# Performance work log

Measured on AMD Instinct MI355X. Metric: run time of the kernel, lower is better.

The kernel has to match this reference:

```python
import jax, jax.numpy as jnp
import numpy as np

STRIDES = (2, 2, 2, 2)
ALPHA = 1.0
NEG_SLOPE = 0.1


def _conv1d(h, w, b, stride):
    # h: (N, C, L), w: (O, I, K) -> (N, O, L_out), VALID padding
    out = jax.lax.conv_general_dilated(
        h, w, window_strides=(stride,), padding='VALID',
        dimension_numbers=('NCH', 'OIH', 'NCH'))
    return out + b[None, :, None]


def setup_inputs() -> dict:
    key = jax.random.key(0)
    ks = jax.random.split(key, 10)
    N, C, L = 256, 128, 1024
    k_sizes = (15, 12, 7, 4)
    inp = {'x': jax.random.normal(ks[0], (N, C, L), dtype=jnp.float32)}
    for i, k in enumerate(k_sizes):
        fan_in = C * k
        scale = 1.0 / np.sqrt(fan_in).astype(np.float32)
        inp[f'w{i+1}'] = jax.random.normal(ks[1 + 2 * i], (C, C, k), dtype=jnp.float32) * scale
        inp[f'b{i+1}'] = jax.random.normal(ks[2 + 2 * i], (C,), dtype=jnp.float32) * 0.01
    D = C * 59  # flattened encoder output: 1024->505->247->121->59
    inp['centers'] = jax.random.normal(ks[9], (64, D), dtype=jnp.float32)
    return inp


def reference(x, w1, b1, w2, b2, w3, b3, w4, b4, centers):
    ws = [(w1, b1), (w2, b2), (w3, b3), (w4, b4)]
    h = x
    for i, ((w, b), s) in enumerate(zip(ws, STRIDES)):
        h = _conv1d(h, w, b, s)
        if i != len(ws) - 1:
            h = jnp.where(h > 0, h, NEG_SLOPE * h)  # LeakyReLU(0.1)
    z = h.reshape(h.shape[0], -1)  # (N, D)
    # squared distances via norm expansion: ||z||^2 + ||c||^2 - 2 z.c
    d2 = (jnp.sum(z * z, axis=1, keepdims=True)
          + jnp.sum(centers * centers, axis=1)[None, :]
          - 2.0 * z @ centers.T)  # (N, K)
    q = 1.0 / (1.0 + d2 / ALPHA)
    q = q ** ((ALPHA + 1.0) / 2.0)
    q = q / jnp.sum(q, axis=1, keepdims=True)
    return q
```

## Files before the change

kernel.cpp:

```cpp
#include <hip/hip_runtime.h>

typedef __bf16 bf16;
typedef __bf16 bf16x4 __attribute__((ext_vector_type(4)));
typedef __bf16 bf16x8 __attribute__((ext_vector_type(8)));
typedef float f32x4 __attribute__((ext_vector_type(4)));

#define CCH 128

__global__ void k_prep_all(const float* __restrict__ w1, const float* __restrict__ w2,
                           const float* __restrict__ w3, const float* __restrict__ w4,
                           const float* __restrict__ cen,
                           bf16* __restrict__ o1, bf16* __restrict__ o2,
                           bf16* __restrict__ o3, bf16* __restrict__ o4,
                           bf16* __restrict__ cbp, float* __restrict__ cc) {
    __shared__ float red[256];
    int tid = threadIdx.x;
    if (blockIdx.x < 2432) {
        int idx = blockIdx.x * 256 + tid;
        const float* src; bf16* dst; int Kw; int r = idx;
        if (r < 15 * 16384) { src = w1; dst = o1; Kw = 15; }
        else if ((r -= 15 * 16384) < 12 * 16384) { src = w2; dst = o2; Kw = 12; }
        else if ((r -= 12 * 16384) < 7 * 16384) { src = w3; dst = o3; Kw = 7; }
        else if ((r -= 7 * 16384) < 4 * 16384) { src = w4; dst = o4; Kw = 4; }
        else return;
        int e = r & 7, lane = (r >> 3) & 63, og = (r >> 9) & 7, c = (r >> 12) & 3, kt = r >> 14;
        int o = og * 16 + (lane & 15);
        int i = c * 32 + (lane >> 4) * 8 + e;
        dst[r] = (bf16)src[(o * 128 + i) * Kw + kt];
    } else {
        int k = blockIdx.x - 2432;
        float s = 0.f;
        for (int idx = tid; idx < 64 * 128; idx += 256) {
            int l = idx >> 7;
            int o = idx & 127;
            float v = (l < 59) ? cen[k * 7552 + o * 59 + l] : 0.f;
            bf16 b = (bf16)v;
            cbp[(size_t)k * 64 * 128 + idx] = b;
            float fv = (float)b;
            s += fv * fv;
        }
        red[tid] = s;
        __syncthreads();
        for (int st = 128; st > 0; st >>= 1) {
            if (tid < st) red[tid] += red[tid + st];
            __syncthreads();
        }
        if (tid == 0) cc[k] = red[0];
    }
}

__global__ __launch_bounds__(256, 4) void k_conv1(
    const float* __restrict__ x, const bf16* __restrict__ wTp,
    const float* __restrict__ bias, bf16* __restrict__ out) {
    constexpr int KW = 15, LT = 128, PH = 2, OUT_ROWS = 512;
    constexpr int P = (LT - 1) * 2 + KW;
    constexpr int KC = 2;
    constexpr int RS = 64;
    constexpr int NLT = LT / 16;
    constexpr int ESE = 136;
    constexpr int SMELE = (P * RS > LT * ESE) ? P * RS : LT * ESE;
    constexpr int NJ = KW * KC;
    __shared__ __align__(16) bf16 smem[SMELE];

    const int n = blockIdx.y;
    const int l0 = blockIdx.x * LT;
    const int p0 = l0 * 2;
    const int tid = threadIdx.x;
    const int wid = tid >> 6;
    const int lane = tid & 63;
    const int quad = lane >> 4;
    const int l15 = lane & 15;
    const int og0 = wid * 2;

    f32x4 acc[2][NLT];
#pragma unroll
    for (int a = 0; a < 2; ++a)
#pragma unroll
        for (int b = 0; b < NLT; ++b) acc[a][b] = (f32x4){0.f, 0.f, 0.f, 0.f};

    bf16x8 afr[2][2];
    const bf16* wbase = wTp + (size_t)lane * 8;
    afr[0][0] = *(const bf16x8*)(wbase + ((size_t)(og0 + 0) << 9));
    afr[0][1] = *(const bf16x8*)(wbase + ((size_t)(og0 + 1) << 9));

    const int cst = tid >> 2;
    const int qw = tid & 3;

#pragma unroll 1
    for (int ph = 0; ph < PH; ++ph) {
        if (ph) __syncthreads();

        const float* bch = x + ((size_t)(n * 128 + ph * 64 + cst)) * 1024;
#pragma unroll 4
        for (int it = 0; it < 17; ++it) {
            int pp = it * 16 + qw * 4;
            int gp = p0 + pp;
            f32x4 t;
            if (gp + 3 < 1024) {
                t = *(const f32x4*)(bch + gp);
            } else {
#pragma unroll
                for (int e = 0; e < 4; ++e) t[e] = (gp + e < 1024) ? bch[gp + e] : 0.f;
            }
#pragma unroll
            for (int e = 0; e < 4; ++e) {
                int ppe = pp + e;
                int sc8 = (((cst >> 3) ^ ((ppe >> 1) & 7)) << 3) | (cst & 7);
                smem[ppe * RS + sc8] = (bf16)t[e];
            }
        }
        __syncthreads();

#pragma unroll 2
        for (int j = 0; j < NJ; ++j) {
            int nj = j + 1, nph = ph;
            if (nj == NJ) { nj = 0; ++nph; }
            if (nph < PH) {
                int kt1 = nj >> 1;
                int c1 = (nj & (KC - 1)) + nph * KC;
                const bf16* wp = wbase + ((size_t)((kt1 * 4 + c1) * 8 + og0) << 9);
                afr[(j + 1) & 1][0] = *(const bf16x8*)(wp);
                afr[(j + 1) & 1][1] = *(const bf16x8*)(wp + 512);
            }
            const int kt = j >> 1;
            const int c16l = (j & (KC - 1)) * 4 + quad;
#pragma unroll
            for (int lt = 0; lt < NLT; ++lt) {
                int p = (lt * 16 + l15) * 2 + kt;
                int sc = c16l ^ ((p >> 1) & 7);
                bf16x8 bfr = *(const bf16x8*)(smem + p * RS + sc * 8);
                acc[0][lt] = __builtin_amdgcn_mfma_f32_16x16x32_bf16(
                    afr[j & 1][0], bfr, acc[0][lt], 0, 0, 0);
                acc[1][lt] = __builtin_amdgcn_mfma_f32_16x16x32_bf16(
                    afr[j & 1][1], bfr, acc[1][lt], 0, 0, 0);
            }
        }
    }

    __syncthreads();
#pragma unroll
    for (int ot = 0; ot < 2; ++ot) {
        const int o0 = wid * 32 + ot * 16 + quad * 4;
        const f32x4 bv = *(const f32x4*)(bias + o0);
#pragma unroll
        for (int lt = 0; lt < NLT; ++lt) {
            const int l = lt * 16 + l15;
            bf16x4 pk;
#pragma unroll
            for (int r = 0; r < 4; ++r) {
                float v = acc[ot][lt][r] + bv[r];
                v = (v > 0.f) ? v : 0.1f * v;
                pk[r] = (bf16)v;
            }
            *(bf16x4*)(smem + l * ESE + o0) = pk;
        }
    }
    __syncthreads();
    constexpr int SNIT = LT * 16 / 256;
    bf16* op = out + ((size_t)n * OUT_ROWS + l0) * CCH;
#pragma unroll
    for (int it = 0; it < SNIT; ++it) {
        int u = tid + it * 256;
        int l = u >> 4;
        int g = u & 15;
        *(bf16x8*)(op + l * CCH + g * 8) = *(const bf16x8*)(smem + l * ESE + g * 8);
    }
}

__global__ __launch_bounds__(512, 1) void k_fused234(
    const bf16* __restrict__ h1g, const bf16* __restrict__ wT2,
    const bf16* __restrict__ wT3, const bf16* __restrict__ wT4,
    const float* __restrict__ b2, const float* __restrict__ b3,
    const float* __restrict__ b4, const bf16* __restrict__ cbp,
    const float* __restrict__ cc, float* __restrict__ out) {
    __shared__ __align__(16) bf16 lds[34048 + 33536];
    __shared__ float d2s[64];
    bf16* sbuf = lds;
    bf16* h2   = lds + 34048;
    bf16* h3   = lds;
    bf16* zmem = lds + 16640;

    const int n = blockIdx.x;
    const int tid = threadIdx.x;
    const int wid = tid >> 6;
    const int lane = tid & 63;
    const int quad = lane >> 4;
    const int l15 = lane & 15;

    if (tid < 96) *(f32x4*)(h2 + 256 * 128 + tid * 8) = (f32x4){0.f, 0.f, 0.f, 0.f};

    {
        const int w4 = wid & 3;
        const int g = wid >> 2;
        const int og0 = w4 * 2;
        const bf16* w2base = wT2 + (size_t)lane * 8;
        constexpr int NJ2 = 48;
#pragma unroll 1
        for (int s = 0; s < 2; ++s) {
            if (s) __syncthreads();
            {
                const bf16* base = h1g + (size_t)n * 512 * 128;
#pragma unroll
                for (int it = 0; it < 9; ++it) {
                    int u = tid + it * 512;
                    if (u < 266 * 16) {
                        int p = u >> 4, c = u & 15;
                        int prow = s * 256 + p; if (prow > 511) prow = 511;
                        bf16x8 t = *(const bf16x8*)(base + (size_t)prow * 128 + c * 8);
                        int sc = (c & 8) | ((c & 7) ^ ((p >> 1) & 7));
                        *(bf16x8*)(sbuf + p * 128 + sc * 8) = t;
                    }
                }
            }
            __syncthreads();

            f32x4 acc[2][4];
#pragma unroll
            for (int a = 0; a < 2; ++a)
#pragma unroll
                for (int b = 0; b < 4; ++b) acc[a][b] = (f32x4){0.f, 0.f, 0.f, 0.f};
            bf16x8 afr[2][2];
            afr[0][0] = *(const bf16x8*)(w2base + ((size_t)og0 << 9));
            afr[0][1] = *(const bf16x8*)(w2base + ((size_t)(og0 + 1) << 9));
#pragma unroll 2
            for (int j = 0; j < NJ2; ++j) {
                if (j + 1 < NJ2) {
                    int kt1 = (j + 1) >> 2, c1 = (j + 1) & 3;
                    const bf16* wp = w2base + ((size_t)((kt1 * 4 + c1) * 8 + og0) << 9);
                    afr[(j + 1) & 1][0] = *(const bf16x8*)(wp);
                    afr[(j + 1) & 1][1] = *(const bf16x8*)(wp + 512);
                }
                int kt = j >> 2;
                int c16l = (j & 3) * 4 + quad;
#pragma unroll
                for (int lt = 0; lt < 4; ++lt) {
                    int p = (g * 64 + lt * 16 + l15) * 2 + kt;
                    int sc = (c16l & 8) | ((c16l & 7) ^ ((p >> 1) & 7));
                    bf16x8 bfr = *(const bf16x8*)(sbuf + p * 128 + sc * 8);
                    acc[0][lt] = __builtin_amdgcn_mfma_f32_16x16x32_bf16(
                        afr[j & 1][0], bfr, acc[0][lt], 0, 0, 0);
                    acc[1][lt] = __builtin_amdgcn_mfma_f32_16x16x32_bf16(
                        afr[j & 1][1], bfr, acc[1][lt], 0, 0, 0);
                }
            }
#pragma unroll
            for (int ot = 0; ot < 2; ++ot) {
                int o0 = (og0 + ot) * 16 + quad * 4;
                f32x4 bv = *(const f32x4*)(b2 + o0);
                int c = o0 >> 3;
#pragma unroll
                for (int lt = 0; lt < 4; ++lt) {
                    int l = s * 128 + g * 64 + lt * 16 + l15;
                    bf16x4 pk;
#pragma unroll
                    for (int r = 0; r < 4; ++r) {
                        float v = acc[ot][lt][r] + bv[r];
                        v = (v > 0.f) ? v : 0.1f * v;
                        pk[r] = (bf16)v;
                    }
                    int sc = (c & 8) | ((c & 7) ^ ((l >> 1) & 7));
                    *(bf16x4*)(h2 + l * 128 + sc * 8 + (o0 & 7)) = pk;
                }
            }
            __syncthreads();
        }
    }

    {
        if (tid < 32) *(f32x4*)(h3 + 128 * 128 + tid * 8) = (f32x4){0.f, 0.f, 0.f, 0.f};
        const int og0 = (wid & 3) * 2;
        const int ph3 = wid >> 2;
        const bf16* w3base = wT3 + (size_t)lane * 8;
        constexpr int NJ3 = 28;
        f32x4 acc[2][4];
#pragma unroll
        for (int a = 0; a < 2; ++a)
#pragma unroll
            for (int b = 0; b < 4; ++b) acc[a][b] = (f32x4){0.f, 0.f, 0.f, 0.f};
        bf16x8 afr[2][2];
        afr[0][0] = *(const bf16x8*)(w3base + ((size_t)og0 << 9));
        afr[0][1] = *(const bf16x8*)(w3base + ((size_t)(og0 + 1) << 9));
#pragma unroll 2
        for (int j = 0; j < NJ3; ++j) {
            if (j + 1 < NJ3) {
                int kt1 = (j + 1) >> 2, c1 = (j + 1) & 3;
                const bf16* wp = w3base + ((size_t)((kt1 * 4 + c1) * 8 + og0) << 9);
                afr[(j + 1) & 1][0] = *(const bf16x8*)(wp);
                afr[(j + 1) & 1][1] = *(const bf16x8*)(wp + 512);
            }
            int kt = j >> 2;
            int c16l = (j & 3) * 4 + quad;
#pragma unroll
            for (int lt = 0; lt < 4; ++lt) {
                int p = (ph3 * 64 + lt * 16 + l15) * 2 + kt;
                int sc = (c16l & 8) | ((c16l & 7) ^ ((p >> 1) & 7));
                bf16x8 bfr = *(const bf16x8*)(h2 + p * 128 + sc * 8);
                acc[0][lt] = __builtin_amdgcn_mfma_f32_16x16x32_bf16(
                    afr[j & 1][0], bfr, acc[0][lt], 0, 0, 0);
                acc[1][lt] = __builtin_amdgcn_mfma_f32_16x16x32_bf16(
                    afr[j & 1][1], bfr, acc[1][lt], 0, 0, 0);
            }
        }
        __syncthreads();
#pragma unroll
        for (int ot = 0; ot < 2; ++ot) {
            int o0 = (og0 + ot) * 16 + quad * 4;
            f32x4 bv = *(const f32x4*)(b3 + o0);
            int c = o0 >> 3;
#pragma unroll
            for (int lt = 0; lt < 4; ++lt) {
                int l = ph3 * 64 + lt * 16 + l15;
                bf16x4 pk;
#pragma unroll
                for (int r = 0; r < 4; ++r) {
                    float v = acc[ot][lt][r] + bv[r];
                    v = (v > 0.f) ? v : 0.1f * v;
                    pk[r] = (bf16)v;
                }
                int sc = (c & 8) | ((c & 7) ^ ((l >> 1) & 7));
                *(bf16x4*)(h3 + l * 128 + sc * 8 + (o0 & 7)) = pk;
            }
        }
    }
    __syncthreads();

    {
        f32x4 acc[4];
#pragma unroll
        for (int b = 0; b < 4; ++b) acc[b] = (f32x4){0.f, 0.f, 0.f, 0.f};
        bf16x8 afr[2];
        const bf16* w4base = wT4 + (size_t)lane * 8;
        afr[0] = *(const bf16x8*)(w4base + ((size_t)wid << 9));
        constexpr int NJ4 = 16;
#pragma unroll 2
        for (int j = 0; j < NJ4; ++j) {
            if (j + 1 < NJ4) {
                int kt1 = (j + 1) >> 2, c1 = (j + 1) & 3;
                afr[(j + 1) & 1] =
                    *(const bf16x8*)(w4base + ((size_t)((kt1 * 4 + c1) * 8 + wid) << 9));
            }
            int kt = j >> 2;
            int c16l = (j & 3) * 4 + quad;
#pragma unroll
            for (int lt = 0; lt < 4; ++lt) {
                int p = (lt * 16 + l15) * 2 + kt;
                int sc = (c16l & 8) | ((c16l & 7) ^ ((p >> 1) & 7));
                bf16x8 bfr = *(const bf16x8*)(h3 + p * 128 + sc * 8);
                acc[lt] = __builtin_amdgcn_mfma_f32_16x16x32_bf16(afr[j & 1], bfr, acc[lt], 0, 0, 0);
            }
        }
        const int o0 = wid * 16 + quad * 4;
        const f32x4 bv = *(const f32x4*)(b4 + o0);
#pragma unroll
        for (int lt = 0; lt < 4; ++lt) {
            const int l = lt * 16 + l15;
            bf16x4 pk;
#pragma unroll
            for (int r = 0; r < 4; ++r) {
                float v = acc[lt][r] + bv[r];
                pk[r] = (l < 59) ? (bf16)v : (bf16)0.f;
            }
            *(bf16x4*)(zmem + l * 136 + o0) = pk;
        }
    }
    __syncthreads();

#pragma unroll 1
    for (int cp = 0; cp < 8; ++cp) {
        const int kc = cp * 8 + wid;
        const bf16* cr = cbp + (size_t)kc * 8192;
        float t = 0.f;
#pragma unroll
        for (int it = 0; it < 16; ++it) {
            int ci = it * 64 + lane;
            int l = ci >> 4;
            int g = ci & 15;
            bf16x8 cv = *(const bf16x8*)(cr + ci * 8);
            bf16x8 zv = *(const bf16x8*)(zmem + l * 136 + g * 8);
#pragma unroll
            for (int e = 0; e < 8; ++e) {
                float zf = (float)zv[e];
                t += zf * (zf - 2.f * (float)cv[e]);
            }
        }
#pragma unroll
        for (int o = 32; o > 0; o >>= 1) t += __shfl_xor(t, o);
        if (lane == 0) d2s[kc] = t + cc[kc];
    }
    __syncthreads();
    if (tid < 64) {
        float q = 1.f / (1.f + d2s[tid]);
        float tot = q;
#pragma unroll
        for (int o = 32; o > 0; o >>= 1) tot += __shfl_xor(tot, o);
        out[n * 64 + tid] = q / tot;
    }
}

extern "C" void kernel_launch(void* const* d_in, const int* in_sizes, int n_in,
                              void* d_out, int out_size, void* d_ws, size_t ws_size,
                              hipStream_t stream) {
    (void)in_sizes; (void)n_in; (void)out_size; (void)ws_size;
    const float* x   = (const float*)d_in[0];
    const float* w1  = (const float*)d_in[1];
    const float* b1  = (const float*)d_in[2];
    const float* w2  = (const float*)d_in[3];
    const float* b2  = (const float*)d_in[4];
    const float* w3  = (const float*)d_in[5];
    const float* b3  = (const float*)d_in[6];
    const float* w4  = (const float*)d_in[7];
    const float* b4  = (const float*)d_in[8];
    const float* cen = (const float*)d_in[9];
    float* out = (float*)d_out;

    char* ws = (char*)d_ws;
    size_t off = 0;
    auto alloc = [&](size_t bytes) -> void* {
        void* p = ws + off;
        off += (bytes + 255) & ~(size_t)255;
        return p;
    };
    bf16* wT1 = (bf16*)alloc((size_t)15 * 16384 * sizeof(bf16));
    bf16* wT2 = (bf16*)alloc((size_t)12 * 16384 * sizeof(bf16));
    bf16* wT3 = (bf16*)alloc((size_t)7 * 16384 * sizeof(bf16));
    bf16* wT4 = (bf16*)alloc((size_t)4 * 16384 * sizeof(bf16));
    bf16* cbp = (bf16*)alloc((size_t)64 * 64 * 128 * sizeof(bf16));
    float* cc = (float*)alloc(64 * sizeof(float));
    bf16* h1  = (bf16*)alloc((size_t)256 * 512 * 128 * sizeof(bf16));
    (void)alloc((size_t)1 << 20);

    k_prep_all<<<2432 + 64, 256, 0, stream>>>(w1, w2, w3, w4, cen,
                                              wT1, wT2, wT3, wT4, cbp, cc);
    k_conv1<<<dim3(4, 256), 256, 0, stream>>>(x, wT1, b1, h1);
    k_fused234<<<256, 512, 0, stream>>>(h1, wT2, wT3, wT4, b2, b3, b4, cbp, cc, out);
}
```

Baseline: 312.4 us.

## Compute cluster distances with MFMA and prefetch second conv2 input half

The per-sample distance stage now uses bf16 MFMA instructions on centers repacked into MFMA fragment layout, replacing a scalar dot-product loop. ||z||^2 is reduced from the conv4 epilogue and ||c||^2 is precomputed separately. The second half of the conv2 input is loaded into registers during the first half's setup, so that global latency overlaps and the load is off the critical path. The costs are extra register pressure from nine prefetched vectors and a larger prep launch to pack the centers.

```diff
diff --git a/kernel.cpp b/kernel.cpp
--- a/kernel.cpp
+++ b/kernel.cpp
@@ -12,11 +12,12 @@
                            const float* __restrict__ cen,
                            bf16* __restrict__ o1, bf16* __restrict__ o2,
                            bf16* __restrict__ o3, bf16* __restrict__ o4,
-                           bf16* __restrict__ cbp, float* __restrict__ cc) {
+                           bf16* __restrict__ cpk, float* __restrict__ cc) {
     __shared__ float red[256];
     int tid = threadIdx.x;
-    if (blockIdx.x < 2432) {
-        int idx = blockIdx.x * 256 + tid;
+    int bid = blockIdx.x;
+    if (bid < 2432) {
+        int idx = bid * 256 + tid;
         const float* src; bf16* dst; int Kw; int r = idx;
         if (r < 15 * 16384) { src = w1; dst = o1; Kw = 15; }
         else if ((r -= 15 * 16384) < 12 * 16384) { src = w2; dst = o2; Kw = 12; }
@@ -27,17 +28,29 @@
         int o = og * 16 + (lane & 15);
         int i = c * 32 + (lane >> 4) * 8 + e;
         dst[r] = (bf16)src[(o * 128 + i) * Kw + kt];
+    } else if (bid < 2432 + 256) {
+        int j = bid - 2432;
+        int l = j >> 2;
+#pragma unroll
+        for (int it = 0; it < 8; ++it) {
+            int u = tid + it * 256;
+            int og = u >> 9, r9 = u & 511;
+            int lane = r9 >> 3, e = r9 & 7;
+            int k = og * 16 + (lane & 15);
+            int oc = (j & 3) * 32 + (lane >> 4) * 8 + e;
+            float v = (l < 59) ? cen[k * 7552 + oc * 59 + l] : 0.f;
+            cpk[(((size_t)(j * 4 + og)) << 9) + r9] = (bf16)v;
+        }
     } else {
-        int k = blockIdx.x - 2432;
+        int k = bid - (2432 + 256);
         float s = 0.f;
-        for (int idx = tid; idx < 64 * 128; idx += 256) {
+        for (int idx = tid; idx < 8192; idx += 256) {
             int l = idx >> 7;
             int o = idx & 127;
-            float v = (l < 59) ? cen[k * 7552 + o * 59 + l] : 0.f;
-            bf16 b = (bf16)v;
-            cbp[(size_t)k * 64 * 128 + idx] = b;
-            float fv = (float)b;
-            s += fv * fv;
+            if (l < 59) {
+                float fv = (float)(bf16)cen[k * 7552 + o * 59 + l];
+                s += fv * fv;
+            }
         }
         red[tid] = s;
         __syncthreads();
@@ -171,10 +184,11 @@
     const bf16* __restrict__ h1g, const bf16* __restrict__ wT2,
     const bf16* __restrict__ wT3, const bf16* __restrict__ wT4,
     const float* __restrict__ b2, const float* __restrict__ b3,
-    const float* __restrict__ b4, const bf16* __restrict__ cbp,
+    const float* __restrict__ b4, const bf16* __restrict__ cpk,
     const float* __restrict__ cc, float* __restrict__ out) {
     __shared__ __align__(16) bf16 lds[34048 + 33536];
-    __shared__ float d2s[64];
+    __shared__ float d2p[2][64];
+    __shared__ float zred[8];
     bf16* sbuf = lds;
     bf16* h2   = lds + 34048;
     bf16* h3   = lds;
@@ -194,26 +208,10 @@
         const int g = wid >> 2;
         const int og0 = w4 * 2;
         const bf16* w2base = wT2 + (size_t)lane * 8;
+        const bf16* base = h1g + (size_t)n * 512 * 128;
         constexpr int NJ2 = 48;
-#pragma unroll 1
-        for (int s = 0; s < 2; ++s) {
-            if (s) __syncthreads();
-            {
-                const bf16* base = h1g + (size_t)n * 512 * 128;
-#pragma unroll
-                for (int it = 0; it < 9; ++it) {
-                    int u = tid + it * 512;
-                    if (u < 266 * 16) {
-                        int p = u >> 4, c = u & 15;
-                        int prow = s * 256 + p; if (prow > 511) prow = 511;
-                        bf16x8 t = *(const bf16x8*)(base + (size_t)prow * 128 + c * 8);
-                        int sc = (c & 8) | ((c & 7) ^ ((p >> 1) & 7));
-                        *(bf16x8*)(sbuf + p * 128 + sc * 8) = t;
-                    }
-                }
-            }
-            __syncthreads();
-
+
+        auto conv2_compute = [&](int s) {
             f32x4 acc[2][4];
 #pragma unroll
             for (int a = 0; a < 2; ++a)
@@ -262,8 +260,44 @@
                     *(bf16x4*)(h2 + l * 128 + sc * 8 + (o0 & 7)) = pk;
                 }
             }
-            __syncthreads();
-        }
+        };
+
+#pragma unroll
+        for (int it = 0; it < 9; ++it) {
+            int u = tid + it * 512;
+            if (u < 266 * 16) {
+                int p = u >> 4, c = u & 15;
+                bf16x8 t = *(const bf16x8*)(base + (size_t)p * 128 + c * 8);
+                int sc = (c & 8) | ((c & 7) ^ ((p >> 1) & 7));
+                *(bf16x8*)(sbuf + p * 128 + sc * 8) = t;
+            }
+        }
+        bf16x8 nb[9];
+#pragma unroll
+        for (int it = 0; it < 9; ++it) {
+            int u = tid + it * 512;
+            if (u < 266 * 16) {
+                int p = u >> 4, c = u & 15;
+                int prow = 256 + p; if (prow > 511) prow = 511;
+                nb[it] = *(const bf16x8*)(base + (size_t)prow * 128 + c * 8);
+            }
+        }
+        __syncthreads();
+
+        conv2_compute(0);
+        __syncthreads();
+#pragma unroll
+        for (int it = 0; it < 9; ++it) {
+            int u = tid + it * 512;
+            if (u < 266 * 16) {
+                int p = u >> 4, c = u & 15;
+                int sc = (c & 8) | ((c & 7) ^ ((p >> 1) & 7));
+                *(bf16x8*)(sbuf + p * 128 + sc * 8) = nb[it];
+            }
+        }
+        __syncthreads();
+        conv2_compute(1);
+        __syncthreads();
     }
 
     {
@@ -351,6 +385,7 @@
         }
         const int o0 = wid * 16 + quad * 4;
         const f32x4 bv = *(const f32x4*)(b4 + o0);
+        float s2 = 0.f;
 #pragma unroll
         for (int lt = 0; lt < 4; ++lt) {
             const int l = lt * 16 + l15;
@@ -359,37 +394,50 @@
             for (int r = 0; r < 4; ++r) {
                 float v = acc[lt][r] + bv[r];
                 pk[r] = (l < 59) ? (bf16)v : (bf16)0.f;
+                float zf = (float)pk[r];
+                s2 += zf * zf;
             }
             *(bf16x4*)(zmem + l * 136 + o0) = pk;
         }
+#pragma unroll
+        for (int o = 32; o > 0; o >>= 1) s2 += __shfl_xor(s2, o);
+        if (lane == 0) zred[wid] = s2;
     }
     __syncthreads();
 
-#pragma unroll 1
-    for (int cp = 0; cp < 8; ++cp) {
-        const int kc = cp * 8 + wid;
-        const bf16* cr = cbp + (size_t)kc * 8192;
-        float t = 0.f;
-#pragma unroll
-        for (int it = 0; it < 16; ++it) {
-            int ci = it * 64 + lane;
-            int l = ci >> 4;
-            int g = ci & 15;
-            bf16x8 cv = *(const bf16x8*)(cr + ci * 8);
-            bf16x8 zv = *(const bf16x8*)(zmem + l * 136 + g * 8);
-#pragma unroll
-            for (int e = 0; e < 8; ++e) {
-                float zf = (float)zv[e];
-                t += zf * (zf - 2.f * (float)cv[e]);
-            }
-        }
-#pragma unroll
-        for (int o = 32; o > 0; o >>= 1) t += __shfl_xor(t, o);
-        if (lane == 0) d2s[kc] = t + cc[kc];
+    {
+        const int og = wid & 3;
+        const int h = wid >> 2;
+        const bf16* cb = cpk + ((size_t)og << 9) + (size_t)lane * 8;
+        f32x4 acc = (f32x4){0.f, 0.f, 0.f, 0.f};
+        const int j0 = h * 128;
+        bf16x8 af[4];
+#pragma unroll
+        for (int q = 0; q < 4; ++q)
+            af[q] = *(const bf16x8*)(cb + ((size_t)(j0 + q) << 11));
+#pragma unroll 4
+        for (int jj = 0; jj < 128; ++jj) {
+            bf16x8 a = af[jj & 3];
+            if (jj + 4 < 128)
+                af[jj & 3] = *(const bf16x8*)(cb + ((size_t)(j0 + jj + 4) << 11));
+            int l = h * 32 + (jj >> 2);
+            int off = (jj & 3) * 32 + quad * 8;
+            bf16x8 b = *(const bf16x8*)(zmem + l * 136 + off);
+            acc = __builtin_amdgcn_mfma_f32_16x16x32_bf16(a, b, acc, 0, 0, 0);
+        }
+        if (l15 == 0) {
+#pragma unroll
+            for (int r = 0; r < 4; ++r) d2p[h][og * 16 + quad * 4 + r] = acc[r];
+        }
     }
     __syncthreads();
+
     if (tid < 64) {
-        float q = 1.f / (1.f + d2s[tid]);
+        float zc = d2p[0][tid] + d2p[1][tid];
+        float z2 = zred[0] + zred[1] + zred[2] + zred[3]
+                 + zred[4] + zred[5] + zred[6] + zred[7];
+        float d2v = z2 + cc[tid] - 2.f * zc;
+        float q = 1.f / (1.f + d2v);
         float tot = q;
 #pragma unroll
         for (int o = 32; o > 0; o >>= 1) tot += __shfl_xor(tot, o);
@@ -424,13 +472,13 @@
     bf16* wT2 = (bf16*)alloc((size_t)12 * 16384 * sizeof(bf16));
     bf16* wT3 = (bf16*)alloc((size_t)7 * 16384 * sizeof(bf16));
     bf16* wT4 = (bf16*)alloc((size_t)4 * 16384 * sizeof(bf16));
-    bf16* cbp = (bf16*)alloc((size_t)64 * 64 * 128 * sizeof(bf16));
+    bf16* cpk = (bf16*)alloc((size_t)1024 * 512 * sizeof(bf16));
     float* cc = (float*)alloc(64 * sizeof(float));
     bf16* h1  = (bf16*)alloc((size_t)256 * 512 * 128 * sizeof(bf16));
     (void)alloc((size_t)1 << 20);
 
-    k_prep_all<<<2432 + 64, 256, 0, stream>>>(w1, w2, w3, w4, cen,
-                                              wT1, wT2, wT3, wT4, cbp, cc);
+    k_prep_all<<<2432 + 256 + 64, 256, 0, stream>>>(w1, w2, w3, w4, cen,
+                                                    wT1, wT2, wT3, wT4, cpk, cc);
     k_conv1<<<dim3(4, 256), 256, 0, stream>>>(x, wT1, b1, h1);
-    k_fused234<<<256, 512, 0, stream>>>(h1, wT2, wT3, wT4, b2, b3, b4, cbp, cc, out);
+    k_fused234<<<256, 512, 0, stream>>>(h1, wT2, wT3, wT4, b2, b3, b4, cpk, cc, out);
 }
```

Measured after the change: 324.3 us. 1.04x slower.
